# Kernel tuning notes

Measured on AMD Instinct MI355X. Metric: run time of the kernel, lower is better.

## Reference

```python
import jax, jax.numpy as jnp
import numpy as np

B, N, E, H = 8, 512, 64, 128


def setup_inputs() -> dict:
    key = jax.random.key(0)
    ks = jax.random.split(key, 9)
    s_in = 1.0 / np.sqrt(2 * E)
    s_h = 1.0 / np.sqrt(H)
    s_e = 1.0 / np.sqrt(E)
    return {
        "X": jax.random.normal(ks[0], (B, N, E), dtype=jnp.float32),
        # cross-sim MLP: Linear(2E,H) -> ReLU -> Linear(H,1) -> Sigmoid
        "Wc1": jax.random.uniform(ks[1], (2 * E, H), jnp.float32, -s_in, s_in),
        "bc1": jax.random.uniform(ks[2], (H,), jnp.float32, -s_in, s_in),
        "Wc2": jax.random.uniform(ks[3], (H, 1), jnp.float32, -s_h, s_h),
        "bc2": jax.random.uniform(ks[4], (1,), jnp.float32, -s_h, s_h),
        # self-sim MLP: Linear(E,H) -> ReLU -> Linear(H,1) -> Sigmoid
        "Ws1": jax.random.uniform(ks[5], (E, H), jnp.float32, -s_e, s_e),
        "bs1": jax.random.uniform(ks[6], (H,), jnp.float32, -s_e, s_e),
        "Ws2": jax.random.uniform(ks[7], (H, 1), jnp.float32, -s_h, s_h),
        "bs2": jax.random.uniform(ks[8], (1,), jnp.float32, -s_h, s_h),
    }


def reference(X, Wc1, bc1, Wc2, bc2, Ws1, bs1, Ws2, bs2):
    b, n, _ = X.shape
    idx_i, idx_j = jnp.triu_indices(n, k=1)  # [P], P = n(n-1)/2

    # gather pairwise features: [B, P, 2E]
    X_i = X[:, idx_i, :]
    X_j = X[:, idx_j, :]
    pair = jnp.concatenate([X_i, X_j], axis=-1)

    # tiny cross-sim MLP -> [B, P]
    h = jax.nn.relu(jnp.einsum("bpe,eh->bph", pair, Wc1) + bc1)
    sim_upper = jax.nn.sigmoid(jnp.einsum("bph,ho->bpo", h, Wc2) + bc2)[..., 0]

    # self-sim MLP on the diagonal -> [B, N]
    hd = jax.nn.relu(jnp.einsum("bne,eh->bnh", X, Ws1) + bs1)
    sim_diag = jax.nn.sigmoid(jnp.einsum("bnh,ho->bno", hd, Ws2) + bs2)[..., 0]

    # scatter into symmetric sim matrix [B, N, N]
    sim = jnp.zeros((b, n, n), dtype=X.dtype)
    sim = sim.at[:, idx_i, idx_j].set(sim_upper)
    sim = sim.at[:, idx_j, idx_i].set(sim_upper)
    diag = jnp.arange(n)
    sim = sim.at[:, diag, diag].set(sim_diag)
    return sim
```

## Files before the change

### kernel.cpp

```cpp
#include <hip/hip_runtime.h>

typedef float v4f __attribute__((ext_vector_type(4)));
typedef float v2f __attribute__((ext_vector_type(2)));

#define NTOK 512
#define EDIM 64
#define HDIM 128
#define NN   (NTOK*NTOK)
#define CPAD 36

__device__ float Ag_buf[8*NTOK*HDIM];
__device__ float Bg_buf[8*NTOK*HDIM];

__device__ __forceinline__ float sigf(float x) {
    return __builtin_amdgcn_rcpf(1.f + __expf(-x));
}

__global__ __launch_bounds__(256) void precomp_kernel(
    const float* __restrict__ X, const float* __restrict__ Wc1, const float* __restrict__ bc1,
    const float* __restrict__ Ws1, const float* __restrict__ bs1,
    const float* __restrict__ Ws2, const float* __restrict__ bs2,
    float* __restrict__ out)
{
    __shared__ float Xs[8*EDIM];
    __shared__ float red[8*132];
    const int t  = threadIdx.x;
    const int g0 = blockIdx.x * 8;
    const int h  = t & 127;
    const int rg = t >> 7;

    for (int i = t; i < 8*EDIM; i += 256) Xs[i] = X[g0*EDIM + i];
    __syncthreads();

    float accA[4] = {0}, accB[4] = {0}, accS[4] = {0};
    #pragma unroll 8
    for (int e = 0; e < EDIM; e++) {
        float wt = Wc1[e*HDIM + h];
        float wb = Wc1[(EDIM+e)*HDIM + h];
        float ws = Ws1[e*HDIM + h];
        #pragma unroll
        for (int r = 0; r < 4; r++) {
            float x = Xs[(rg*4 + r)*EDIM + e];
            accA[r] = fmaf(x, wt, accA[r]);
            accB[r] = fmaf(x, wb, accB[r]);
            accS[r] = fmaf(x, ws, accS[r]);
        }
    }
    const float b1 = bc1[h], s1 = bs1[h], w2 = Ws2[h];
    #pragma unroll
    for (int r = 0; r < 4; r++) {
        const int row = rg*4 + r;
        Ag_buf[(g0+row)*HDIM + h] = accA[r];
        Bg_buf[(g0+row)*HDIM + h] = accB[r] + b1;
        float hd = fmaxf(accS[r] + s1, 0.f);
        red[row*132 + h] = hd * w2;
    }
    __syncthreads();
    if (t < 8) {
        const float* rr = red + t*132;
        float s = 0.f;
        #pragma unroll
        for (int i = 0; i < HDIM/4; i++) {
            v4f v = *(const v4f*)(rr + 4*i);
            s += v[0] + v[1] + v[2] + v[3];
        }
        float val = sigf(s + bs2[0]);
        int g = g0 + t;
        int b = g >> 9, n = g & 511;
        out[b*NN + n*NTOK + n] = val;
    }
}

__global__ __launch_bounds__(256) void pair_kernel(
    const float* __restrict__ Wc2, const float* __restrict__ bc2,
    float* __restrict__ out)
{
    __shared__ float RowT[64*HDIM];
    __shared__ float ColT[HDIM*CPAD];

    const int t = threadIdx.x;
    const int b = blockIdx.y;
    const int u = blockIdx.x;
    int tr, tc, half;
    if (u < 56) {
        int p = u >> 1; half = u & 1;
        tr = 0; int rem = p;
        while (rem >= 7 - tr) { rem -= 7 - tr; tr++; }
        tc = tr + 1 + rem;
    } else {
        int d = (u - 56) >> 1; half = u & 1; tr = d; tc = d;
    }
    const int r0 = tr*64, c0 = tc*64 + half*32;
    const bool isdiag = (tr == tc);

    const float* Rsrc = Ag_buf + (b*NTOK + r0)*HDIM;
    const float* Csrc = Bg_buf + (b*NTOK + c0)*HDIM;

    {
        const int hv = t & 31;
        for (int k = t >> 5; k < 64; k += 8) {
            const int sw = 4*(hv ^ (k & 31));
            *(v4f*)(RowT + k*HDIM + sw) = *(const v4f*)(Rsrc + k*HDIM + 4*hv);
        }
        for (int c = t >> 5; c < 32; c += 8) {
            #pragma unroll
            for (int e = 0; e < 4; e++) {
                int h = hv + 32*e;
                ColT[h*CPAD + c] = Csrc[c*HDIM + h];
            }
        }
    }
    __syncthreads();

    const int w  = t >> 6;
    const int wr = w & 1, wc = w >> 1;
    const int l  = t & 63;
    const int ri = l & 15, cj = l >> 4;
    const int row0 = 32*wr + ri;
    const int ccol = 16*wc + 4*cj;

    const int rb0 = row0*HDIM,      rm0 = row0 & 31;
    const int rb1 = (row0+16)*HDIM, rm1 = (row0+16) & 31;

    v2f acc[2][2] = {{{0,0},{0,0}},{{0,0},{0,0}}};
    for (int hq = 0; hq < HDIM/4; hq++) {
        const v4f w4 = *(const v4f*)(Wc2 + 4*hq);
        v4f ra0 = *(const v4f*)(RowT + rb0 + 4*(hq ^ rm0));
        v4f ra1 = *(const v4f*)(RowT + rb1 + 4*(hq ^ rm1));
        #pragma unroll
        for (int hh = 0; hh < 4; hh++) {
            const v4f cb = *(const v4f*)(ColT + (4*hq+hh)*CPAD + ccol);
            v2f clo; clo[0] = cb[0]; clo[1] = cb[1];
            v2f chi; chi[0] = cb[2]; chi[1] = cb[3];
            const float wv = w4[hh];
            v2f wv2; wv2[0] = wv; wv2[1] = wv;
            v2f z = {0.f, 0.f};
            {
                v2f a2; a2[0] = ra0[hh]; a2[1] = ra0[hh];
                v2f y0 = __builtin_elementwise_max(a2 + clo, z);
                v2f y1 = __builtin_elementwise_max(a2 + chi, z);
                acc[0][0] += y0 * wv2;
                acc[0][1] += y1 * wv2;
            }
            {
                v2f a2; a2[0] = ra1[hh]; a2[1] = ra1[hh];
                v2f y0 = __builtin_elementwise_max(a2 + clo, z);
                v2f y1 = __builtin_elementwise_max(a2 + chi, z);
                acc[1][0] += y0 * wv2;
                acc[1][1] += y1 * wv2;
            }
        }
    }

    const float bb = bc2[0];
    float* outb = out + b*NN;
    float sv[2][4];
    #pragma unroll
    for (int uu = 0; uu < 2; uu++) {
        sv[uu][0] = sigf(acc[uu][0][0] + bb);
        sv[uu][1] = sigf(acc[uu][0][1] + bb);
        sv[uu][2] = sigf(acc[uu][1][0] + bb);
        sv[uu][3] = sigf(acc[uu][1][1] + bb);
    }

    if (!isdiag) {
        #pragma unroll
        for (int uu = 0; uu < 2; uu++) {
            int r = r0 + row0 + 16*uu;
            v4f p; p[0] = sv[uu][0]; p[1] = sv[uu][1]; p[2] = sv[uu][2]; p[3] = sv[uu][3];
            *(v4f*)(outb + r*NTOK + c0 + ccol) = p;
        }
        __syncthreads();
        float* Tb = ColT;
        #pragma unroll
        for (int uu = 0; uu < 2; uu++)
            #pragma unroll
            for (int v = 0; v < 4; v++)
                Tb[(ccol + v)*68 + row0 + 16*uu] = sv[uu][v];
        __syncthreads();
        const int q = t >> 3, x0 = (t & 7) * 8;
        const float* src = Tb + q*68 + x0;
        v4f a0 = *(const v4f*)src;
        v4f a1 = *(const v4f*)(src + 4);
        float* drow = outb + (c0 + q)*NTOK + r0 + x0;
        *(v4f*)drow = a0;
        *(v4f*)(drow + 4) = a1;
    } else {
        #pragma unroll
        for (int uu = 0; uu < 2; uu++) {
            int r = r0 + row0 + 16*uu;
            #pragma unroll
            for (int v = 0; v < 4; v++) {
                int c = c0 + ccol + v;
                if (r < c) {
                    outb[r*NTOK + c] = sv[uu][v];
                    outb[c*NTOK + r] = sv[uu][v];
                }
            }
        }
    }
}

extern "C" void kernel_launch(void* const* d_in, const int* in_sizes, int n_in,
                              void* d_out, int out_size, void* d_ws, size_t ws_size,
                              hipStream_t stream) {
    const float* X   = (const float*)d_in[0];
    const float* Wc1 = (const float*)d_in[1];
    const float* bc1 = (const float*)d_in[2];
    const float* Wc2 = (const float*)d_in[3];
    const float* bc2 = (const float*)d_in[4];
    const float* Ws1 = (const float*)d_in[5];
    const float* bs1 = (const float*)d_in[6];
    const float* Ws2 = (const float*)d_in[7];
    const float* bs2 = (const float*)d_in[8];
    float* out = (float*)d_out;

    (void)d_ws; (void)ws_size;

    precomp_kernel<<<dim3(4096/8), dim3(256), 0, stream>>>(X, Wc1, bc1, Ws1, bs1, Ws2, bs2, out);
    pair_kernel<<<dim3(72, 8), dim3(256), 0, stream>>>(Wc2, bc2, out);
}
```

Before: 102.4 us.

## Split hidden-dim reduction across warps with larger per-thread pair tiles

Each wavefront now owns a quarter of the hidden dimension and computes all 64x32 pair outputs for that slice, with each thread holding a 4x8 tile instead of 2x4. Partial sums are then reduced across the four wavefronts through padded shared memory before the sigmoid. The goal is more register-level reuse of row and column operands per LDS load, which cuts LDS traffic in the inner loop. The cost is an extra shared-memory reduction pass, more barriers, and higher register pressure from the larger accumulator tile.

```diff
diff --git a/kernel.cpp b/kernel.cpp
--- a/kernel.cpp
+++ b/kernel.cpp
@@ -8,6 +8,8 @@
 #define HDIM 128
 #define NN   (NTOK*NTOK)
 #define CPAD 36
+#define PROW 33
+#define PPLANE (64*PROW)
 
 __device__ float Ag_buf[8*NTOK*HDIM];
 __device__ float Bg_buf[8*NTOK*HDIM];
@@ -75,8 +77,9 @@
     const float* __restrict__ Wc2, const float* __restrict__ bc2,
     float* __restrict__ out)
 {
-    __shared__ float RowT[64*HDIM];
+    __shared__ float RowP[4*PPLANE];
     __shared__ float ColT[HDIM*CPAD];
+    float* RowT = RowP;
 
     const int t = threadIdx.x;
     const int b = blockIdx.y;
@@ -113,70 +116,94 @@
     __syncthreads();
 
     const int w  = t >> 6;
-    const int wr = w & 1, wc = w >> 1;
     const int l  = t & 63;
-    const int ri = l & 15, cj = l >> 4;
-    const int row0 = 32*wr + ri;
-    const int ccol = 16*wc + 4*cj;
-
-    const int rb0 = row0*HDIM,      rm0 = row0 & 31;
-    const int rb1 = (row0+16)*HDIM, rm1 = (row0+16) & 31;
-
-    v2f acc[2][2] = {{{0,0},{0,0}},{{0,0},{0,0}}};
-    for (int hq = 0; hq < HDIM/4; hq++) {
+    const int ri = l & 15;
+    const int cj = l >> 4;
+    const int ccol = 8*cj;
+
+    int rbase[4], rmask[4];
+    #pragma unroll
+    for (int k = 0; k < 4; k++) {
+        rbase[k] = (ri + 16*k)*HDIM;
+        rmask[k] = (ri + 16*k) & 31;
+    }
+
+    v2f acc[4][4];
+    #pragma unroll
+    for (int k = 0; k < 4; k++)
+        #pragma unroll
+        for (int v = 0; v < 4; v++) { acc[k][v][0] = 0.f; acc[k][v][1] = 0.f; }
+
+    #pragma unroll 2
+    for (int i = 0; i < 8; i++) {
+        const int hq = 8*w + i;
         const v4f w4 = *(const v4f*)(Wc2 + 4*hq);
-        v4f ra0 = *(const v4f*)(RowT + rb0 + 4*(hq ^ rm0));
-        v4f ra1 = *(const v4f*)(RowT + rb1 + 4*(hq ^ rm1));
+        v4f ra[4];
+        #pragma unroll
+        for (int k = 0; k < 4; k++)
+            ra[k] = *(const v4f*)(RowT + rbase[k] + 4*(hq ^ rmask[k]));
         #pragma unroll
         for (int hh = 0; hh < 4; hh++) {
-            const v4f cb = *(const v4f*)(ColT + (4*hq+hh)*CPAD + ccol);
-            v2f clo; clo[0] = cb[0]; clo[1] = cb[1];
-            v2f chi; chi[0] = cb[2]; chi[1] = cb[3];
+            const float* cp = ColT + (4*hq + hh)*CPAD + ccol;
+            v4f cb0 = *(const v4f*)cp;
+            v4f cb1 = *(const v4f*)(cp + 4);
+            v2f c01; c01[0] = cb0[0]; c01[1] = cb0[1];
+            v2f c23; c23[0] = cb0[2]; c23[1] = cb0[3];
+            v2f c45; c45[0] = cb1[0]; c45[1] = cb1[1];
+            v2f c67; c67[0] = cb1[2]; c67[1] = cb1[3];
             const float wv = w4[hh];
             v2f wv2; wv2[0] = wv; wv2[1] = wv;
             v2f z = {0.f, 0.f};
-            {
-                v2f a2; a2[0] = ra0[hh]; a2[1] = ra0[hh];
-                v2f y0 = __builtin_elementwise_max(a2 + clo, z);
-                v2f y1 = __builtin_elementwise_max(a2 + chi, z);
-                acc[0][0] += y0 * wv2;
-                acc[0][1] += y1 * wv2;
+            #pragma unroll
+            for (int k = 0; k < 4; k++) {
+                v2f a2; a2[0] = ra[k][hh]; a2[1] = ra[k][hh];
+                acc[k][0] += __builtin_elementwise_max(a2 + c01, z) * wv2;
+                acc[k][1] += __builtin_elementwise_max(a2 + c23, z) * wv2;
+                acc[k][2] += __builtin_elementwise_max(a2 + c45, z) * wv2;
+                acc[k][3] += __builtin_elementwise_max(a2 + c67, z) * wv2;
             }
-            {
-                v2f a2; a2[0] = ra1[hh]; a2[1] = ra1[hh];
-                v2f y0 = __builtin_elementwise_max(a2 + clo, z);
-                v2f y1 = __builtin_elementwise_max(a2 + chi, z);
-                acc[1][0] += y0 * wv2;
-                acc[1][1] += y1 * wv2;
-            }
-        }
-    }
-
+        }
+    }
+    __syncthreads();
+
+    {
+        float* Pb = RowP + w*PPLANE;
+        #pragma unroll
+        for (int k = 0; k < 4; k++) {
+            float* pr = Pb + (ri + 16*k)*PROW + ccol;
+            pr[0] = acc[k][0][0]; pr[1] = acc[k][0][1];
+            pr[2] = acc[k][1][0]; pr[3] = acc[k][1][1];
+            pr[4] = acc[k][2][0]; pr[5] = acc[k][2][1];
+            pr[6] = acc[k][3][0]; pr[7] = acc[k][3][1];
+        }
+    }
+    __syncthreads();
+
+    const int frow = t >> 2;
+    const int fc0  = (t & 3) * 8;
     const float bb = bc2[0];
+    float sv[8];
+    #pragma unroll
+    for (int j = 0; j < 8; j++) {
+        const int idx = frow*PROW + fc0 + j;
+        float s = RowP[idx] + RowP[PPLANE + idx]
+                + RowP[2*PPLANE + idx] + RowP[3*PPLANE + idx];
+        sv[j] = sigf(s + bb);
+    }
+
     float* outb = out + b*NN;
-    float sv[2][4];
-    #pragma unroll
-    for (int uu = 0; uu < 2; uu++) {
-        sv[uu][0] = sigf(acc[uu][0][0] + bb);
-        sv[uu][1] = sigf(acc[uu][0][1] + bb);
-        sv[uu][2] = sigf(acc[uu][1][0] + bb);
-        sv[uu][3] = sigf(acc[uu][1][1] + bb);
-    }
-
     if (!isdiag) {
-        #pragma unroll
-        for (int uu = 0; uu < 2; uu++) {
-            int r = r0 + row0 + 16*uu;
-            v4f p; p[0] = sv[uu][0]; p[1] = sv[uu][1]; p[2] = sv[uu][2]; p[3] = sv[uu][3];
-            *(v4f*)(outb + r*NTOK + c0 + ccol) = p;
-        }
-        __syncthreads();
+        {
+            float* drow = outb + (r0 + frow)*NTOK + c0 + fc0;
+            v4f p0; p0[0] = sv[0]; p0[1] = sv[1]; p0[2] = sv[2]; p0[3] = sv[3];
+            v4f p1; p1[0] = sv[4]; p1[1] = sv[5]; p1[2] = sv[6]; p1[3] = sv[7];
+            *(v4f*)drow = p0;
+            *(v4f*)(drow + 4) = p1;
+        }
         float* Tb = ColT;
         #pragma unroll
-        for (int uu = 0; uu < 2; uu++)
-            #pragma unroll
-            for (int v = 0; v < 4; v++)
-                Tb[(ccol + v)*68 + row0 + 16*uu] = sv[uu][v];
+        for (int j = 0; j < 8; j++)
+            Tb[(fc0 + j)*68 + frow] = sv[j];
         __syncthreads();
         const int q = t >> 3, x0 = (t & 7) * 8;
         const float* src = Tb + q*68 + x0;
@@ -187,15 +214,11 @@
         *(v4f*)(drow + 4) = a1;
     } else {
         #pragma unroll
-        for (int uu = 0; uu < 2; uu++) {
-            int r = r0 + row0 + 16*uu;
-            #pragma unroll
-            for (int v = 0; v < 4; v++) {
-                int c = c0 + ccol + v;
-                if (r < c) {
-                    outb[r*NTOK + c] = sv[uu][v];
-                    outb[c*NTOK + r] = sv[uu][v];
-                }
+        for (int j = 0; j < 8; j++) {
+            int r = r0 + frow, c = c0 + fc0 + j;
+            if (r < c) {
+                outb[r*NTOK + c] = sv[j];
+                outb[c*NTOK + r] = sv[j];
             }
         }
     }
```

New measurement: 101.7 us. About the same (-0.7%).
